# Kernel optimization log

Measured on AMD Instinct MI355X. Metric: run time of the kernel, lower is better.

Reference implementation:

```python
import jax, jax.numpy as jnp
import numpy as np

B, T, F, H = 256, 128, 256, 512

def _unif(key, shape, fan_in):
    stv = 1.0 / np.sqrt(fan_in)
    return jax.random.uniform(key, shape, jnp.float32, -stv, stv)

def setup_inputs() -> dict:
    key = jax.random.key(0)
    ks = jax.random.split(key, 20)
    x = jax.random.normal(ks[0], (B, T, F), jnp.float32)
    mask = (jax.random.uniform(ks[1], (B, T, F)) < 0.8).astype(jnp.float32)
    deltas = jax.random.uniform(ks[2], (B, T, F), jnp.float32) * 5.0
    return {
        'x': x, 'mask': mask, 'deltas': deltas,
        'W_gh': _unif(ks[3], (H, F), F), 'b_gh': jnp.zeros((H,), jnp.float32),
        'w_gx': _unif(ks[4], (F,), F), 'b_gx': jnp.zeros((F,), jnp.float32),
        'W_hist': _unif(ks[5], (F, H), H), 'b_hist': jnp.zeros((F,), jnp.float32),
        'W_fr': _unif(ks[6], (F, F), F), 'b_fr': jnp.zeros((F,), jnp.float32),
        'W_comb': _unif(ks[7], (F, 2 * F), 2 * F), 'b_comb': jnp.zeros((F,), jnp.float32),
        'W_ih': _unif(ks[8], (4 * H, 2 * F), 2 * F), 'b_ih': jnp.zeros((4 * H,), jnp.float32),
        'W_hh': _unif(ks[9], (4 * H, H), H), 'b_hh': jnp.zeros((4 * H,), jnp.float32),
    }

def reference(x, mask, deltas, W_gh, b_gh, w_gx, b_gx, W_hist, b_hist,
              W_fr, b_fr, W_comb, b_comb, W_ih, b_ih, W_hh, b_hh):
    dtype = x.dtype
    Fdim = x.shape[2]
    W_fr_m = W_fr * (1.0 - jnp.eye(Fdim, dtype=dtype))

    def step(carry, inp):
        h, c, loss = carry
        x_t, m_t, d_t = inp  # each [B, F]
        gamma_h = jnp.exp(-jax.nn.relu(d_t @ W_gh.T + b_gh))       # [B, H]
        h = h * gamma_h
        x_h = h @ W_hist.T + b_hist                                 # [B, F]
        x_r = m_t * x_t + (1.0 - m_t) * x_h
        xu = x_r @ W_fr_m.T + b_fr                                  # [B, F]
        gamma_x = jnp.exp(-jax.nn.relu(d_t * w_gx + b_gx))          # diag Decay
        beta = jax.nn.sigmoid(jnp.concatenate([gamma_x, m_t], axis=1) @ W_comb.T + b_comb)
        x_comb = beta * xu + (1.0 - beta) * x_h
        # MAE on observed entries, per step, accumulated
        loss = loss + jnp.sum(jnp.abs(x_comb - x_t) * m_t) / (jnp.sum(m_t) + 1e-12)
        x_imp = m_t * x_t + (1.0 - m_t) * x_comb
        rnn_in = jnp.concatenate([x_imp, m_t], axis=1)              # [B, 2F]
        gates = rnn_in @ W_ih.T + b_ih + h @ W_hh.T + b_hh          # [B, 4H]
        i_g, f_g, g_g, o_g = jnp.split(gates, 4, axis=1)
        i_g = jax.nn.sigmoid(i_g); f_g = jax.nn.sigmoid(f_g)
        g_g = jnp.tanh(g_g);       o_g = jax.nn.sigmoid(o_g)
        c = f_g * c + i_g * g_g
        h = o_g * jnp.tanh(c)
        return (h, c, loss), (x_imp, x_comb)

    Bdim, Hdim = x.shape[0], W_hh.shape[1]
    init = (jnp.zeros((Bdim, Hdim), dtype), jnp.zeros((Bdim, Hdim), dtype), jnp.zeros((), dtype))
    xs = (x.transpose(1, 0, 2), mask.transpose(1, 0, 2), deltas.transpose(1, 0, 2))
    (h, c, x_loss), (x_imp_seq, rec_seq) = jax.lax.scan(step, init, xs)
    x_imp = x_imp_seq.transpose(1, 0, 2)          # [B, T, F]
    reconstruction = rec_seq.transpose(1, 0, 2)   # [B, T, F]
    kl = jnp.zeros((), dtype)                     # non-bayesian
    return x_imp, reconstruction, h, x_loss, kl
```

## Files before the change

### kernel.cpp

```cpp
#include <hip/hip_runtime.h>
#include <hip/hip_bf16.h>

typedef float f32x4 __attribute__((ext_vector_type(4)));
typedef __bf16 bf16x8 __attribute__((ext_vector_type(8)));
typedef short s16x8 __attribute__((ext_vector_type(8)));
typedef unsigned short u16;
typedef unsigned long long u64;
typedef unsigned char u8;

constexpr int Bb = 256, Tt = 128, Ff = 256, Hh = 512;
constexpr int TF = Tt * Ff;
constexpr long OFF_RECON = (long)Bb * Tt * Ff;
constexpr long OFF_H     = 2L * Bb * Tt * Ff;
constexpr long OFF_LOSS  = OFF_H + (long)Bb * Hh;

__device__ inline float sigf(float v){ return 1.f / (1.f + expf(-v)); }
__device__ inline u16 f2b(float f){
  unsigned u = __float_as_uint(f);
  u += 0x7fffu + ((u >> 16) & 1u);
  return (u16)(u >> 16);
}
__device__ inline float b2f(u16 b){ return __uint_as_float(((unsigned)b) << 16); }

__device__ inline unsigned f2e4_sw(float f){
  unsigned u = __float_as_uint(f);
  unsigned s = (u >> 24) & 0x80u;
  int e = (int)((u >> 23) & 0xff) - 127;
  unsigned m = u & 0x7fffffu;
  if (((u >> 23) & 0xff) == 0xff) return s | 0x7e;
  if (e > 8 || (e == 8 && m > 0x600000)) return s | 0x7e;
  if (e < -10) return s;
  if (e >= -6) {
    unsigned keep = m >> 20, rest = m & 0xfffffu;
    keep += (rest > 0x80000u) || (rest == 0x80000u && (keep & 1));
    unsigned ee = (unsigned)(e + 7);
    if (keep == 8) { keep = 0; ee += 1; }
    if (ee >= 16) return s | 0x7e;
    return s | (ee << 3) | keep;
  }
  unsigned full = (1u << 23) | m;
  int shift = 20 + (-6 - e);
  unsigned keep = full >> shift;
  unsigned rest = full & ((1u << shift) - 1u);
  unsigned half = 1u << (shift - 1);
  keep += (rest > half) || (rest == half && (keep & 1));
  return s | keep;
}
__device__ inline unsigned f2e4(float f){
#if __has_builtin(__builtin_amdgcn_cvt_pk_fp8_f32)
  return (unsigned)__builtin_amdgcn_cvt_pk_fp8_f32(f, f, 0, false) & 0xffu;
#else
  return f2e4_sw(f);
#endif
}
__device__ inline unsigned pk2e4(float a, float b){
#if __has_builtin(__builtin_amdgcn_cvt_pk_fp8_f32)
  return (unsigned)__builtin_amdgcn_cvt_pk_fp8_f32(a, b, 0, false) & 0xffffu;
#else
  return f2e4_sw(a) | (f2e4_sw(b) << 8);
#endif
}

__device__ inline f32x4 mfma16(bf16x8 a, bf16x8 b, f32x4 c){
  return __builtin_amdgcn_mfma_f32_16x16x32_bf16(a, b, c, 0, 0, 0);
}
__device__ inline f32x4 mfma8(u64 a, u64 b, f32x4 c){
  return __builtin_amdgcn_mfma_f32_16x16x32_fp8_fp8((long)a, (long)b, c, 0, 0, 0);
}
__device__ inline bf16x8 ldb8(const u16* p){ return *reinterpret_cast<const bf16x8*>(p); }
__device__ inline bf16x8 cvt8(const float* p){
  const float4 a = ((const float4*)p)[0], b = ((const float4*)p)[1];
  s16x8 r;
  r[0]=f2b(a.x); r[1]=f2b(a.y); r[2]=f2b(a.z); r[3]=f2b(a.w);
  r[4]=f2b(b.x); r[5]=f2b(b.y); r[6]=f2b(b.z); r[7]=f2b(b.w);
  return __builtin_bit_cast(bf16x8, r);
}

enum { M_GH, M_BETA };

struct P {
  const float *x, *mask, *deltas;
  const float *b_gh, *w_gx, *b_gx, *b_comb;
  const u16 *Wgh, *Wcomb;
  u16 *gammah, *beta;
};

template<int MODE>
__global__ __launch_bounds__(256) void gk(P p)
{
  constexpr int K = (MODE==M_GH) ? 256 : 512;
  const int lane = threadIdx.x & 63;
  const int w = threadIdx.x >> 6;
  const int m0 = blockIdx.y*64 + (w>>1)*32;
  const int n0 = blockIdx.x*64 + (w&1)*32;
  const int fr = lane & 15;
  const int kg = (lane >> 4) << 3;

  f32x4 acc[2][2] = {};
  for (int k = 0; k < K; k += 32) {
    const int kk = k + kg;
    bf16x8 a[2], b[2];
    #pragma unroll
    for (int r = 0; r < 2; ++r) {
      const int mr = m0 + 16*r + fr;
      if constexpr (MODE == M_GH) {
        a[r] = cvt8(p.deltas + (size_t)mr*256 + kk);
      } else {
        if (kk < 256) {
          const float4 d0 = *(const float4*)(p.deltas + (size_t)mr*256 + kk);
          const float4 d1 = *(const float4*)(p.deltas + (size_t)mr*256 + kk + 4);
          const float4 w0 = *(const float4*)(p.w_gx + kk);
          const float4 w1 = *(const float4*)(p.w_gx + kk + 4);
          const float4 g0 = *(const float4*)(p.b_gx + kk);
          const float4 g1 = *(const float4*)(p.b_gx + kk + 4);
          s16x8 v;
          v[0]=f2b(expf(-fmaxf(d0.x*w0.x+g0.x,0.f)));
          v[1]=f2b(expf(-fmaxf(d0.y*w0.y+g0.y,0.f)));
          v[2]=f2b(expf(-fmaxf(d0.z*w0.z+g0.z,0.f)));
          v[3]=f2b(expf(-fmaxf(d0.w*w0.w+g0.w,0.f)));
          v[4]=f2b(expf(-fmaxf(d1.x*w1.x+g1.x,0.f)));
          v[5]=f2b(expf(-fmaxf(d1.y*w1.y+g1.y,0.f)));
          v[6]=f2b(expf(-fmaxf(d1.z*w1.z+g1.z,0.f)));
          v[7]=f2b(expf(-fmaxf(d1.w*w1.w+g1.w,0.f)));
          a[r] = __builtin_bit_cast(bf16x8, v);
        } else {
          a[r] = cvt8(p.mask + (size_t)mr*256 + (kk-256));
        }
      }
    }
    #pragma unroll
    for (int cc = 0; cc < 2; ++cc) {
      const int nr = n0 + 16*cc + fr;
      if constexpr (MODE == M_GH) b[cc] = ldb8(p.Wgh   + (size_t)nr*256 + kk);
      else                        b[cc] = ldb8(p.Wcomb + (size_t)nr*512 + kk);
    }
    #pragma unroll
    for (int r = 0; r < 2; ++r)
      #pragma unroll
      for (int cc = 0; cc < 2; ++cc)
        acc[r][cc] = mfma16(a[r], b[cc], acc[r][cc]);
  }

  #pragma unroll
  for (int r = 0; r < 2; ++r)
    #pragma unroll
    for (int cc = 0; cc < 2; ++cc)
      #pragma unroll
      for (int q = 0; q < 4; ++q) {
        const int m = m0 + 16*r + (lane>>4)*4 + q;
        const int n = n0 + 16*cc + (lane&15);
        const size_t tb = (size_t)(m & 127)*256 + (m >> 7);
        if constexpr (MODE == M_GH) {
          float v = expf(-fmaxf(acc[r][cc][q] + p.b_gh[n], 0.f));
          p.gammah[tb*512 + n] = f2b(v);
        } else {
          float v = sigf(acc[r][cc][q] + p.b_comb[n]);
          p.beta[tb*256 + n] = f2b(v);
        }
      }
}

constexpr int CV_TOT = 131072+131072+65536+131072;
__global__ __launch_bounds__(256) void k_conv(
    const float* Wgh, const float* Whist, const float* Wfr, const float* Wcomb,
    u16* ogh, u16* ohist, u16* ofr, u16* ocomb)
{
  int i = blockIdx.x*256 + threadIdx.x;
  if (i >= CV_TOT) return;
  int j = i;
  if (j < 131072) { ogh[j] = f2b(Wgh[j]); return; }       j -= 131072;
  if (j < 131072) { ohist[j] = f2b(Whist[j]); return; }   j -= 131072;
  if (j < 65536)  { ofr[j] = ((j>>8)==(j&255)) ? (u16)0 : f2b(Wfr[j]); return; } j -= 65536;
  ocomb[j] = f2b(Wcomb[j]);
}

__global__ __launch_bounds__(256) void k_conv8(
    const float* Wih, const float* Whh, u8* oih, u8* ohh)
{
  int i = blockIdx.x*256 + threadIdx.x;
  if (i < 524288) {
    ((u16*)oih)[i] = (u16)pk2e4(Wih[2*i], Wih[2*i+1]);
  } else {
    int j = i - 524288;
    ((u16*)ohh)[j] = (u16)pk2e4(Whh[2*j], Whh[2*j+1]);
  }
}

__global__ __launch_bounds__(256) void k_den(const float* __restrict__ mask,
                                             float* den, u8* mask8)
{
  const int t = blockIdx.x;
  const int f = threadIdx.x;
  float s = 0.f;
  for (int b = 0; b < Bb; ++b) {
    float mv = mask[(size_t)b*TF + (size_t)t*256 + f];
    s += mv;
    mask8[((size_t)t*256 + b)*256 + f] = (u8)f2e4(mv);
  }
  __shared__ float red[4];
  #pragma unroll
  for (int o = 32; o; o >>= 1) s += __shfl_down(s, o);
  if ((f & 63) == 0) red[f >> 6] = s;
  __syncthreads();
  if (f == 0) den[t] = red[0]+red[1]+red[2]+red[3];
}

__global__ void k_final(const float* num, const float* den, float* out)
{
  if (threadIdx.x < 64) {
    int t = threadIdx.x;
    float s = num[t]/(den[t]+1e-12f) + num[t+64]/(den[t+64]+1e-12f);
    #pragma unroll
    for (int o = 32; o; o >>= 1) s += __shfl_down(s, o);
    if (t == 0) { out[OFF_LOSS] = s; out[OFF_LOSS+1] = 0.f; }
  }
}

struct PSP {
  const float *x, *mask;
  const float *b_hist, *b_fr, *b_ih, *b_hh;
  const u16 *Whist, *Wfr, *gammah, *beta;
  const u8 *Wih8, *Whh8, *mask8;
  u16 *hb0, *hb1; u8 *h80, *h81;
  float *num, *out;
  unsigned *flags; int *xcc;
};

__global__ __launch_bounds__(1024, 4) void k_loopP(PSP p)
{
  extern __shared__ char smem[];
  u8*    whh_s  = (u8*)smem;
  u16*   h_s    = (u16*)(smem + 131072);
  float* pre_s  = (float*)(smem + 131072);
  u16*   xr_s   = (u16*)(smem + 147968);
  u8*    ximp_s = (u8*)(smem + 156416);
  __shared__ int s_fast;

  const int tid = threadIdx.x, lane = tid & 63, w = tid >> 6;
  const int fr = lane & 15, kg = (lane >> 4) << 3;
  const int bid = blockIdx.x;
  const int slab = bid & 15, cg = bid >> 4;
  const int m0 = slab*16, hc0 = cg*64;

  if (tid == 0) {
    unsigned xv;
    asm volatile("s_getreg_b32 %0, hwreg(HW_REG_XCC_ID)" : "=s"(xv));
    __hip_atomic_store(p.xcc + bid, (int)(xv & 15u) + 1, __ATOMIC_RELAXED, __HIP_MEMORY_SCOPE_AGENT);
    int v0 = 0, ok = 1;
    #pragma unroll 1
    for (int j = 0; j < 8; ++j) {
      int v; unsigned spin = 0;
      do {
        v = __hip_atomic_load(p.xcc + slab + 16*j, __ATOMIC_RELAXED, __HIP_MEMORY_SCOPE_AGENT);
        if (v) break;
        __builtin_amdgcn_s_sleep(8);
      } while (++spin < (1u<<22));
      if (j == 0) v0 = v;
      ok &= (v != 0) && (v == v0);
    }
    s_fast = ok;
  }

  for (int i = tid; i < 8192; i += 1024) {
    const int row = i >> 5;
    const int kk  = (i & 31) << 4;
    const int g = row >> 6, c = row & 63;
    const float4 v = *(const float4*)(p.Whh8 + ((size_t)(g*512 + hc0 + c) << 9) + kk);
    *(float4*)(whh_s + ((size_t)row << 9) + (kk ^ ((row & 7) << 4))) = v;
  }
  __syncthreads();
  const int fast = s_fast;

  const int nA0 = w * 16;
  const float bh  = p.b_hist[nA0 + fr];
  const float bfv = p.b_fr  [nA0 + fr];
  const int gB = w & 3, qh = w >> 2;
  float bsum[4];
  #pragma unroll
  for (int g = 0; g < 4; ++g)
    bsum[g] = p.b_ih[g*512 + hc0 + lane] + p.b_hh[g*512 + hc0 + lane];
  float c0 = 0.f;

  for (int t = 0; t < Tt; ++t) {
    const u16* hr  = (t & 1) ? p.hb1 : p.hb0;
    u16*       hw  = (t & 1) ? p.hb0 : p.hb1;
    const u8*  h8r = (t & 1) ? p.h81 : p.h80;
    u8*        h8w = (t & 1) ? p.h80 : p.h81;

    float mmv[4], xxv[4]; u16 betv[4];
    #pragma unroll
    for (int q = 0; q < 4; ++q) {
      const int row = (lane>>4)*4 + q;
      const int n   = nA0 + fr;
      const size_t gi = (size_t)(m0+row)*TF + (size_t)t*256 + n;
      xxv[q] = p.x[gi];
      mmv[q] = p.mask[gi];
      betv[q] = p.beta[((size_t)t*256 + m0+row)*256 + n];
    }
    u16 gnv = 0;
    if (t < Tt-1)
      gnv = p.gammah[((size_t)(t+1)*256 + m0 + w)*512 + hc0 + lane];

    if (t > 0) {
      if (w == 0 && lane < 8) {
        const unsigned tgt = (unsigned)t;
        unsigned* mf = p.flags + (size_t)(slab + 16*lane)*16;
        unsigned spin = 0;
        if (fast) {
          while (__hip_atomic_load(mf, __ATOMIC_RELAXED, __HIP_MEMORY_SCOPE_AGENT) < tgt
                 && spin < (1u<<24)) { __builtin_amdgcn_s_sleep(8); ++spin; }
        } else {
          while (__hip_atomic_load(mf, __ATOMIC_ACQUIRE, __HIP_MEMORY_SCOPE_AGENT) < tgt
                 && spin < (1u<<24)) { __builtin_amdgcn_s_sleep(8); ++spin; }
        }
      }
      __syncthreads();
      __builtin_amdgcn_sched_barrier(0);
    }

    {
      bf16x8 hv;
      const u16* src = hr + (size_t)(m0 + w)*512 + lane*8;
      asm volatile("global_load_dwordx4 %0, %1, off sc0\n\ts_waitcnt vmcnt(0)"
                   : "=v"(hv) : "v"(src) : "memory");
      *(bf16x8*)(h_s + w*520 + lane*8) = hv;
    }
    __syncthreads();

    f32x4 acc = {};
    #pragma unroll
    for (int k = 0; k < 16; ++k) {
      bf16x8 a = *(const bf16x8*)(h_s + fr*520 + k*32 + kg);
      bf16x8 b = ldb8(p.Whist + (size_t)(nA0 + fr)*512 + k*32 + kg);
      acc = mfma16(a, b, acc);
    }
    float xhv[4];
    #pragma unroll
    for (int q = 0; q < 4; ++q) {
      const int row = (lane>>4)*4 + q;
      const int n   = nA0 + fr;
      const float v = acc[q] + bh;
      xhv[q] = v;
      xr_s[row*264 + n] = f2b(mmv[q]*xxv[q] + (1.f-mmv[q])*v);
    }
    __syncthreads();

    f32x4 acc2 = {};
    #pragma unroll
    for (int k = 0; k < 8; ++k) {
      bf16x8 a = *(const bf16x8*)(xr_s + fr*264 + k*32 + kg);
      bf16x8 b = ldb8(p.Wfr + (size_t)(nA0 + fr)*256 + k*32 + kg);
      acc2 = mfma16(a, b, acc2);
    }
    float xcv[4], xiv[4], lnum = 0.f;
    #pragma unroll
    for (int q = 0; q < 4; ++q) {
      const int row = (lane>>4)*4 + q;
      const int n   = nA0 + fr;
      const float xu  = acc2[q] + bfv;
      const float bet = b2f(betv[q]);
      const float xc  = bet*xu + (1.f-bet)*xhv[q];
      const float xi  = mmv[q]*xxv[q] + (1.f-mmv[q])*xc;
      ximp_s[row*264 + n] = (u8)f2e4(xi);
      xcv[q] = xc; xiv[q] = xi;
      lnum += fabsf(xc - xxv[q])*mmv[q];
    }
    if (cg == 0) {
      #pragma unroll
      for (int o = 32; o; o >>= 1) lnum += __shfl_down(lnum, o);
      if (lane == 0) atomicAdd(p.num + t, lnum);
    }
    __syncthreads();

    u64 a8[16];
    {
      const u8* h8b = h8r + (size_t)(m0 + fr)*512 + kg;
      #pragma unroll
      for (int i = 0; i < 16; ++i) {
        const u8* pa = h8b + i*32;
        asm volatile("global_load_dwordx2 %0, %1, off sc0" : "=&v"(a8[i]) : "v"(pa));
      }
    }
    f32x4 ag = {};
    #pragma unroll
    for (int k = 0; k < 8; ++k) {
      const u64 a = *(const u64*)(ximp_s + (size_t)fr*264 + k*32 + kg);
      const u64 b = *(const u64*)(p.Wih8 + (size_t)(gB*512 + hc0 + qh*16 + fr)*512 + k*32 + kg);
      ag = mfma8(a, b, ag);
    }
    #pragma unroll
    for (int k = 0; k < 8; ++k) {
      const u64 a = *(const u64*)(p.mask8 + ((size_t)t*256 + m0 + fr)*256 + k*32 + kg);
      const u64 b = *(const u64*)(p.Wih8 + (size_t)(gB*512 + hc0 + qh*16 + fr)*512 + 256 + k*32 + kg);
      ag = mfma8(a, b, ag);
    }
    asm volatile("s_waitcnt vmcnt(0)" ::: "memory");
    __builtin_amdgcn_sched_barrier(0);
    {
      const int wrow = gB*64 + qh*16 + fr;
      const int wsw  = (wrow & 7) << 4;
      #pragma unroll
      for (int k = 0; k < 16; ++k) {
        const u64 b = *(const u64*)(whh_s + ((size_t)wrow << 9) + ((k*32 + kg) ^ wsw));
        ag = mfma8(a8[k], b, ag);
      }
    }
    #pragma unroll
    for (int q = 0; q < 4; ++q) {
      const int row = (lane>>4)*4 + q;
      pre_s[(gB*16 + row)*66 + qh*16 + fr] = ag[q];
    }
    __syncthreads();

    {
      const float pi = pre_s[(0*16 + w)*66 + lane] + bsum[0];
      const float pf = pre_s[(1*16 + w)*66 + lane] + bsum[1];
      const float pg = pre_s[(2*16 + w)*66 + lane] + bsum[2];
      const float po = pre_s[(3*16 + w)*66 + lane] + bsum[3];
      const float cv = sigf(pf)*c0 + sigf(pi)*tanhf(pg);
      c0 = cv;
      const float hv = sigf(po)*tanhf(cv);
      const int idx = (m0+w)*512 + hc0 + lane;
      if (t == Tt-1) {
        __builtin_nontemporal_store(hv, p.out + OFF_H + idx);
      } else {
        const float hd = hv * b2f(gnv);
        hw[idx]  = f2b(hd);
        h8w[idx] = (u8)f2e4(hd);
      }
    }

    if (t < Tt-1) {
      asm volatile("s_waitcnt vmcnt(0)" ::: "memory");
      __syncthreads();
      if (tid == 0) {
        if (fast)
          __hip_atomic_store(p.flags + (size_t)bid*16, (unsigned)(t+1),
                             __ATOMIC_RELAXED, __HIP_MEMORY_SCOPE_AGENT);
        else
          __hip_atomic_store(p.flags + (size_t)bid*16, (unsigned)(t+1),
                             __ATOMIC_RELEASE, __HIP_MEMORY_SCOPE_AGENT);
      }
    }

    if (cg == 0) {
      #pragma unroll
      for (int q = 0; q < 4; ++q) {
        const int row = (lane>>4)*4 + q;
        const int n   = nA0 + fr;
        const size_t gi = (size_t)(m0+row)*TF + (size_t)t*256 + n;
        __builtin_nontemporal_store(xcv[q], p.out + OFF_RECON + gi);
        __builtin_nontemporal_store(xiv[q], p.out + gi);
      }
    }
  }
}

extern "C" void kernel_launch(void* const* d_in, const int* in_sizes, int n_in,
                              void* d_out, int out_size, void* d_ws, size_t ws_size,
                              hipStream_t stream)
{
  char* wsb = (char*)d_ws;
  unsigned* flags = (unsigned*)(wsb + 0);
  int*      xcc   = (int*)(wsb + 8192);
  float*    num   = (float*)(wsb + 8704);
  u16*  hb0    = (u16*)(wsb + 9216);
  u8*   h80    = (u8*)(wsb + 271360);
  u16*  hb1    = (u16*)(wsb + 402432);
  u8*   h81    = (u8*)(wsb + 664576);
  float* den   = (float*)(wsb + 795648);
  u8*   mask8  = (u8*)(wsb + 796160);
  u16*  beta   = (u16*)(wsb + 9184768);
  u16*  gammah = (u16*)(wsb + 25961984);
  u16*  Whist  = (u16*)(wsb + 59516416);
  u16*  Wfr    = (u16*)(wsb + 59778560);
  u16*  Wgh    = (u16*)(wsb + 59909632);
  u16*  Wcomb  = (u16*)(wsb + 60171776);
  u8*   Wih8   = (u8*)(wsb + 60433920);
  u8*   Whh8   = (u8*)(wsb + 61482496);

  hipMemsetAsync(d_ws, 0, 402432, stream);

  k_conv<<<dim3((CV_TOT+255)/256), dim3(256), 0, stream>>>(
      (const float*)d_in[3], (const float*)d_in[7], (const float*)d_in[9],
      (const float*)d_in[11], Wgh, Whist, Wfr, Wcomb);
  k_conv8<<<dim3(4096), dim3(256), 0, stream>>>(
      (const float*)d_in[13], (const float*)d_in[15], Wih8, Whh8);
  k_den<<<dim3(128), dim3(256), 0, stream>>>((const float*)d_in[1], den, mask8);

  P p{};
  p.x = (const float*)d_in[0];  p.mask = (const float*)d_in[1];
  p.deltas = (const float*)d_in[2];
  p.b_gh = (const float*)d_in[4];  p.w_gx = (const float*)d_in[5];
  p.b_gx = (const float*)d_in[6];  p.b_comb = (const float*)d_in[12];
  p.Wgh = Wgh; p.Wcomb = Wcomb;
  p.gammah = gammah; p.beta = beta;
  gk<M_GH><<<dim3(8, 512), dim3(256), 0, stream>>>(p);
  gk<M_BETA><<<dim3(4, 512), dim3(256), 0, stream>>>(p);

  PSP ps{};
  ps.x = (const float*)d_in[0];  ps.mask = (const float*)d_in[1];
  ps.b_hist = (const float*)d_in[8];  ps.b_fr = (const float*)d_in[10];
  ps.b_ih = (const float*)d_in[14];   ps.b_hh = (const float*)d_in[16];
  ps.Whist = Whist; ps.Wfr = Wfr; ps.gammah = gammah; ps.beta = beta;
  ps.Wih8 = Wih8; ps.Whh8 = Whh8; ps.mask8 = mask8;
  ps.hb0 = hb0; ps.hb1 = hb1; ps.h80 = h80; ps.h81 = h81;
  ps.num = num; ps.out = (float*)d_out;
  ps.flags = flags; ps.xcc = xcc;

  (void)hipFuncSetAttribute((const void*)k_loopP,
      hipFuncAttributeMaxDynamicSharedMemorySize, 160640);
  k_loopP<<<dim3(128), dim3(1024), 160640, stream>>>(ps);

  k_final<<<dim3(1), dim3(64), 0, stream>>>(num, den, (float*)d_out);
}
```

Before: 4.886 ms.

## Drop fp8 hidden buffers, convert h in LDS, stream Whh from global

The separate fp8 copy of the hidden state in global memory is removed. The fp8 A operand for the recurrent matmul is now built from the bf16 hidden state already held in LDS. The 128KB LDS copy of Whh8 is dropped, so Whh8 is read from global (L2) on every step, and dynamic shared memory becomes small static buffers. Every wave now polls the step flags itself with a shorter sleep, which removes a block-wide barrier, and the loss reduction moves after the flag release. This cuts per-step global writes and synchronisation latency, but adds repeated L2 traffic for Whh and extra conversion ALU work on the critical path.

```diff
diff --git a/kernel.cpp b/kernel.cpp
--- a/kernel.cpp
+++ b/kernel.cpp
@@ -74,6 +74,11 @@
   r[0]=f2b(a.x); r[1]=f2b(a.y); r[2]=f2b(a.z); r[3]=f2b(a.w);
   r[4]=f2b(b.x); r[5]=f2b(b.y); r[6]=f2b(b.z); r[7]=f2b(b.w);
   return __builtin_bit_cast(bf16x8, r);
+}
+__device__ inline u64 cvt_h8(const u16* hs){
+  unsigned lo = pk2e4(b2f(hs[0]), b2f(hs[1])) | (pk2e4(b2f(hs[2]), b2f(hs[3])) << 16);
+  unsigned hi = pk2e4(b2f(hs[4]), b2f(hs[5])) | (pk2e4(b2f(hs[6]), b2f(hs[7])) << 16);
+  return (u64)lo | ((u64)hi << 32);
 }
 
 enum { M_GH, M_BETA };
@@ -221,19 +226,17 @@
   const float *b_hist, *b_fr, *b_ih, *b_hh;
   const u16 *Whist, *Wfr, *gammah, *beta;
   const u8 *Wih8, *Whh8, *mask8;
-  u16 *hb0, *hb1; u8 *h80, *h81;
+  u16 *hb0, *hb1;
   float *num, *out;
   unsigned *flags; int *xcc;
 };
 
 __global__ __launch_bounds__(1024, 4) void k_loopP(PSP p)
 {
-  extern __shared__ char smem[];
-  u8*    whh_s  = (u8*)smem;
-  u16*   h_s    = (u16*)(smem + 131072);
-  float* pre_s  = (float*)(smem + 131072);
-  u16*   xr_s   = (u16*)(smem + 147968);
-  u8*    ximp_s = (u8*)(smem + 156416);
+  __shared__ u16  h_s[16*520];
+  __shared__ u16  xr_s[16*264];
+  __shared__ u8   ximp_s[16*264];
+  __shared__ float pre_s[4*16*66];
   __shared__ int s_fast;
 
   const int tid = threadIdx.x, lane = tid & 63, w = tid >> 6;
@@ -260,14 +263,6 @@
     }
     s_fast = ok;
   }
-
-  for (int i = tid; i < 8192; i += 1024) {
-    const int row = i >> 5;
-    const int kk  = (i & 31) << 4;
-    const int g = row >> 6, c = row & 63;
-    const float4 v = *(const float4*)(p.Whh8 + ((size_t)(g*512 + hc0 + c) << 9) + kk);
-    *(float4*)(whh_s + ((size_t)row << 9) + (kk ^ ((row & 7) << 4))) = v;
-  }
   __syncthreads();
   const int fast = s_fast;
 
@@ -284,8 +279,6 @@
   for (int t = 0; t < Tt; ++t) {
     const u16* hr  = (t & 1) ? p.hb1 : p.hb0;
     u16*       hw  = (t & 1) ? p.hb0 : p.hb1;
-    const u8*  h8r = (t & 1) ? p.h81 : p.h80;
-    u8*        h8w = (t & 1) ? p.h80 : p.h81;
 
     float mmv[4], xxv[4]; u16 betv[4];
     #pragma unroll
@@ -302,22 +295,20 @@
       gnv = p.gammah[((size_t)(t+1)*256 + m0 + w)*512 + hc0 + lane];
 
     if (t > 0) {
-      if (w == 0 && lane < 8) {
+      if (lane < 8) {
         const unsigned tgt = (unsigned)t;
-        unsigned* mf = p.flags + (size_t)(slab + 16*lane)*16;
+        const unsigned* mf = p.flags + (size_t)(slab + 16*lane)*16;
         unsigned spin = 0;
         if (fast) {
           while (__hip_atomic_load(mf, __ATOMIC_RELAXED, __HIP_MEMORY_SCOPE_AGENT) < tgt
-                 && spin < (1u<<24)) { __builtin_amdgcn_s_sleep(8); ++spin; }
+                 && spin < (1u<<24)) { __builtin_amdgcn_s_sleep(2); ++spin; }
         } else {
           while (__hip_atomic_load(mf, __ATOMIC_ACQUIRE, __HIP_MEMORY_SCOPE_AGENT) < tgt
-                 && spin < (1u<<24)) { __builtin_amdgcn_s_sleep(8); ++spin; }
+                 && spin < (1u<<24)) { __builtin_amdgcn_s_sleep(2); ++spin; }
         }
       }
-      __syncthreads();
       __builtin_amdgcn_sched_barrier(0);
     }
-
     {
       bf16x8 hv;
       const u16* src = hr + (size_t)(m0 + w)*512 + lane*8;
@@ -365,22 +356,8 @@
       xcv[q] = xc; xiv[q] = xi;
       lnum += fabsf(xc - xxv[q])*mmv[q];
     }
-    if (cg == 0) {
-      #pragma unroll
-      for (int o = 32; o; o >>= 1) lnum += __shfl_down(lnum, o);
-      if (lane == 0) atomicAdd(p.num + t, lnum);
-    }
     __syncthreads();
 
-    u64 a8[16];
-    {
-      const u8* h8b = h8r + (size_t)(m0 + fr)*512 + kg;
-      #pragma unroll
-      for (int i = 0; i < 16; ++i) {
-        const u8* pa = h8b + i*32;
-        asm volatile("global_load_dwordx2 %0, %1, off sc0" : "=&v"(a8[i]) : "v"(pa));
-      }
-    }
     f32x4 ag = {};
     #pragma unroll
     for (int k = 0; k < 8; ++k) {
@@ -394,16 +371,11 @@
       const u64 b = *(const u64*)(p.Wih8 + (size_t)(gB*512 + hc0 + qh*16 + fr)*512 + 256 + k*32 + kg);
       ag = mfma8(a, b, ag);
     }
-    asm volatile("s_waitcnt vmcnt(0)" ::: "memory");
-    __builtin_amdgcn_sched_barrier(0);
-    {
-      const int wrow = gB*64 + qh*16 + fr;
-      const int wsw  = (wrow & 7) << 4;
-      #pragma unroll
-      for (int k = 0; k < 16; ++k) {
-        const u64 b = *(const u64*)(whh_s + ((size_t)wrow << 9) + ((k*32 + kg) ^ wsw));
-        ag = mfma8(a8[k], b, ag);
-      }
+    #pragma unroll
+    for (int k = 0; k < 16; ++k) {
+      const u64 a = cvt_h8(h_s + fr*520 + k*32 + kg);
+      const u64 b = *(const u64*)(p.Whh8 + (size_t)(gB*512 + hc0 + qh*16 + fr)*512 + k*32 + kg);
+      ag = mfma8(a, b, ag);
     }
     #pragma unroll
     for (int q = 0; q < 4; ++q) {
@@ -425,8 +397,7 @@
         __builtin_nontemporal_store(hv, p.out + OFF_H + idx);
       } else {
         const float hd = hv * b2f(gnv);
-        hw[idx]  = f2b(hd);
-        h8w[idx] = (u8)f2e4(hd);
+        hw[idx] = f2b(hd);
       }
     }
 
@@ -445,6 +416,9 @@
 
     if (cg == 0) {
       #pragma unroll
+      for (int o = 32; o; o >>= 1) lnum += __shfl_down(lnum, o);
+      if (lane == 0) atomicAdd(p.num + t, lnum);
+      #pragma unroll
       for (int q = 0; q < 4; ++q) {
         const int row = (lane>>4)*4 + q;
         const int n   = nA0 + fr;
@@ -465,21 +439,19 @@
   int*      xcc   = (int*)(wsb + 8192);
   float*    num   = (float*)(wsb + 8704);
   u16*  hb0    = (u16*)(wsb + 9216);
-  u8*   h80    = (u8*)(wsb + 271360);
-  u16*  hb1    = (u16*)(wsb + 402432);
-  u8*   h81    = (u8*)(wsb + 664576);
-  float* den   = (float*)(wsb + 795648);
-  u8*   mask8  = (u8*)(wsb + 796160);
-  u16*  beta   = (u16*)(wsb + 9184768);
-  u16*  gammah = (u16*)(wsb + 25961984);
-  u16*  Whist  = (u16*)(wsb + 59516416);
-  u16*  Wfr    = (u16*)(wsb + 59778560);
-  u16*  Wgh    = (u16*)(wsb + 59909632);
-  u16*  Wcomb  = (u16*)(wsb + 60171776);
-  u8*   Wih8   = (u8*)(wsb + 60433920);
-  u8*   Whh8   = (u8*)(wsb + 61482496);
-
-  hipMemsetAsync(d_ws, 0, 402432, stream);
+  u16*  hb1    = (u16*)(wsb + 271360);
+  float* den   = (float*)(wsb + 533504);
+  u8*   mask8  = (u8*)(wsb + 534016);
+  u16*  beta   = (u16*)(wsb + 8922624);
+  u16*  gammah = (u16*)(wsb + 25699840);
+  u16*  Whist  = (u16*)(wsb + 59254272);
+  u16*  Wfr    = (u16*)(wsb + 59516416);
+  u16*  Wgh    = (u16*)(wsb + 59647488);
+  u16*  Wcomb  = (u16*)(wsb + 59909632);
+  u8*   Wih8   = (u8*)(wsb + 60171776);
+  u8*   Whh8   = (u8*)(wsb + 61220352);
+
+  hipMemsetAsync(d_ws, 0, 271360, stream);
 
   k_conv<<<dim3((CV_TOT+255)/256), dim3(256), 0, stream>>>(
       (const float*)d_in[3], (const float*)d_in[7], (const float*)d_in[9],
@@ -504,13 +476,10 @@
   ps.b_ih = (const float*)d_in[14];   ps.b_hh = (const float*)d_in[16];
   ps.Whist = Whist; ps.Wfr = Wfr; ps.gammah = gammah; ps.beta = beta;
   ps.Wih8 = Wih8; ps.Whh8 = Whh8; ps.mask8 = mask8;
-  ps.hb0 = hb0; ps.hb1 = hb1; ps.h80 = h80; ps.h81 = h81;
+  ps.hb0 = hb0; ps.hb1 = hb1;
   ps.num = num; ps.out = (float*)d_out;
   ps.flags = flags; ps.xcc = xcc;
-
-  (void)hipFuncSetAttribute((const void*)k_loopP,
-      hipFuncAttributeMaxDynamicSharedMemorySize, 160640);
-  k_loopP<<<dim3(128), dim3(1024), 160640, stream>>>(ps);
+  k_loopP<<<dim3(128), dim3(1024), 0, stream>>>(ps);
 
   k_final<<<dim3(1), dim3(64), 0, stream>>>(num, den, (float*)d_out);
 }
```

After: 4.245 ms. 1.15x faster.
